# Kernel optimization log

Hardware: AMD Instinct MI355X
Metric: run time of the kernel (lower is better)

The kernel has to match this reference:

```python
import jax, jax.numpy as jnp
import numpy as np

I, H, O = 8, 32, 1  # input_size, hidden_size, output_size


def setup_inputs() -> dict:
    key = jax.random.key(0)
    ks = jax.random.split(key, 7)
    B, T = 4096, 256
    s_ih = 1.0 / np.sqrt(H)
    inp = {
        "x": jax.random.normal(ks[0], (B, T, I), dtype=jnp.float32),
        # PyTorch nn.LSTM params, gate order [i, f, g, o]
        "W_ih": jax.random.uniform(ks[1], (4 * H, I), minval=-s_ih, maxval=s_ih, dtype=jnp.float32),
        "W_hh": jax.random.uniform(ks[2], (4 * H, H), minval=-s_ih, maxval=s_ih, dtype=jnp.float32),
        "b_ih": jax.random.uniform(ks[3], (4 * H,), minval=-s_ih, maxval=s_ih, dtype=jnp.float32),
        "b_hh": jax.random.uniform(ks[4], (4 * H,), minval=-s_ih, maxval=s_ih, dtype=jnp.float32),
        # nn.Linear(H, O)
        "W_out": jax.random.uniform(ks[5], (O, H), minval=-s_ih, maxval=s_ih, dtype=jnp.float32),
        "b_out": jax.random.uniform(ks[6], (O,), minval=-s_ih, maxval=s_ih, dtype=jnp.float32),
    }
    return inp


def _lstm_last_h(x, W_ih, W_hh, b_ih, b_hh):
    B = x.shape[0]
    # Precompute input projections for all steps: [T, B, 4H]
    x_proj = jnp.einsum("bti,gi->tbg", x, W_ih) + (b_ih + b_hh)
    h0 = jnp.zeros((B, H), dtype=x.dtype)
    c0 = jnp.zeros((B, H), dtype=x.dtype)

    def step(carry, xp):
        h, c = carry
        z = xp + h @ W_hh.T  # [B, 4H]
        i = jax.nn.sigmoid(z[:, 0 * H:1 * H])
        f = jax.nn.sigmoid(z[:, 1 * H:2 * H])
        g = jnp.tanh(z[:, 2 * H:3 * H])
        o = jax.nn.sigmoid(z[:, 3 * H:4 * H])
        c = f * c + i * g
        h = o * jnp.tanh(c)
        return (h, c), None

    (hT, _), _ = jax.lax.scan(step, (h0, c0), x_proj)
    return hT  # equals out[:, -1, :] for unidirectional batch_first LSTM


def reference(x, W_ih, W_hh, b_ih, b_hh, W_out, b_out):
    hT = _lstm_last_h(x, W_ih, W_hh, b_ih, b_hh)
    return hT @ W_out.T + b_out  # [B, O]
```

## Files before the change

kernel.cpp:

```cpp
#include <hip/hip_runtime.h>


#define T_LEN 256
#define LOG2E 1.4426950408889634f

typedef short bf16x8 __attribute__((ext_vector_type(8)));
typedef float f32x4 __attribute__((ext_vector_type(4)));

static __device__ inline short f2bf_rne(float f) {
    union { float f; unsigned u; } v; v.f = f;
    unsigned u = v.u;
    return (short)((u + 0x7FFFu + ((u >> 16) & 1u)) >> 16);
}
static __device__ inline short f2bf_fast(float f) {
    union { float f; unsigned u; } v; v.f = f;
    return (short)((v.u + 0x8000u) >> 16);
}
static __device__ inline unsigned pack_bf2(float a, float b) {
    union { float f; unsigned u; } x, y; x.f = a; y.f = b;
    return ((x.u + 0x8000u) >> 16) | ((y.u + 0x8000u) & 0xFFFF0000u);
}
static __device__ inline float bf2f(short s) {
    union { unsigned u; float f; } v;
    v.u = ((unsigned)(unsigned short)s) << 16;
    return v.f;
}

__global__ __launch_bounds__(256) void lstm_kernel(
    const float* __restrict__ x, const float* __restrict__ W_ih,
    const float* __restrict__ W_hh, const float* __restrict__ b_ih,
    const float* __restrict__ b_hh, const float* __restrict__ W_out,
    const float* __restrict__ b_out, float* __restrict__ out)
{
    __shared__ __attribute__((aligned(16))) short h_lds[2][16 * 40];

    const int tid  = threadIdx.x;
    const int w    = tid >> 6;
    const int lane = tid & 63;
    const int L    = lane & 15;
    const int q    = lane >> 4;
    const int row0 = blockIdx.x * 16;

    bf16x8 whh[2], wih[2];
    f32x4  bias[2];
#pragma unroll
    for (int e = 0; e < 2; ++e) {
        const int   n = 32 * (L & 3) + 8 * (L >> 2) + 2 * w + e;
        const float s = ((L & 3) == 2 ? 2.f * LOG2E : LOG2E);
        const float* src = W_hh + n * 32 + q * 8;
        bf16x8 fr;
#pragma unroll
        for (int j = 0; j < 8; ++j) fr[j] = f2bf_rne(src[j] * s);
        whh[e] = fr;
        bf16x8 gr = (bf16x8){0,0,0,0,0,0,0,0};
        if (q == 0) {
            const float* s2 = W_ih + n * 8;
#pragma unroll
            for (int j = 0; j < 8; ++j) gr[j] = f2bf_rne(s2[j] * s);
        }
        wih[e] = gr;
        f32x4 bb;
#pragma unroll
        for (int r = 0; r < 4; ++r) {
            const int   nr = 32 * r + 8 * q + 2 * w + e;
            const float sr = (r == 2 ? 2.f * LOG2E : LOG2E);
            bb[r] = (b_ih[nr] + b_hh[nr]) * sr;
        }
        bias[e] = bb;
    }

    const float4* xv = (const float4*)x;
    const size_t  xb = (size_t)(row0 + L) * (T_LEN * 8 / 4);
    float4 xr0[2] = {{0,0,0,0},{0,0,0,0}}, xr1[2] = {{0,0,0,0},{0,0,0,0}};
    bf16x8 xf0 = (bf16x8){0,0,0,0,0,0,0,0};
    if (q == 0) {
        const float4 a = xv[xb + 0], b = xv[xb + 1];
        xf0[0] = f2bf_fast(a.x); xf0[1] = f2bf_fast(a.y);
        xf0[2] = f2bf_fast(a.z); xf0[3] = f2bf_fast(a.w);
        xf0[4] = f2bf_fast(b.x); xf0[5] = f2bf_fast(b.y);
        xf0[6] = f2bf_fast(b.z); xf0[7] = f2bf_fast(b.w);
        xr0[1] = xv[xb + 2]; xr1[1] = xv[xb + 3];
        xr0[0] = xv[xb + 4]; xr1[0] = xv[xb + 5];
    }

    f32x4 zx[2];
    zx[0] = __builtin_amdgcn_mfma_f32_16x16x32_bf16(wih[0], xf0, bias[0], 0, 0, 0);
    zx[1] = __builtin_amdgcn_mfma_f32_16x16x32_bf16(wih[1], xf0, bias[1], 0, 0, 0);

    bf16x8 hfrag = (bf16x8){0,0,0,0,0,0,0,0};
    float c0 = 0.f, c1 = 0.f;

#pragma unroll 2
    for (int t = 0; t < T_LEN; ++t) {
        const int nxt = (t + 1) & 1;

        const f32x4 a0 = __builtin_amdgcn_mfma_f32_16x16x32_bf16(whh[0], hfrag, zx[0], 0, 0, 0);
        const f32x4 a1 = __builtin_amdgcn_mfma_f32_16x16x32_bf16(whh[1], hfrag, zx[1], 0, 0, 0);

        float h0, h1;
        {
            const float ei = __builtin_amdgcn_exp2f(fminf(-a0[0], 40.f));
            const float ef = __builtin_amdgcn_exp2f(fminf(-a0[1], 40.f));
            const float eg = __builtin_amdgcn_exp2f(fminf(-a0[2], 40.f));
            const float eo = __builtin_amdgcn_exp2f(fminf(-a0[3], 40.f));
            const float fv = __builtin_amdgcn_rcpf(1.f + ef);
            const float ig = (1.f - eg) * __builtin_amdgcn_rcpf((1.f + ei) * (1.f + eg));
            c0 = fmaf(fv, c0, ig);
            const float ec = __builtin_amdgcn_exp2f(fminf(c0 * (-2.f * LOG2E), 40.f));
            h0 = (1.f - ec) * __builtin_amdgcn_rcpf((1.f + eo) * (1.f + ec));
        }
        {
            const float ei = __builtin_amdgcn_exp2f(fminf(-a1[0], 40.f));
            const float ef = __builtin_amdgcn_exp2f(fminf(-a1[1], 40.f));
            const float eg = __builtin_amdgcn_exp2f(fminf(-a1[2], 40.f));
            const float eo = __builtin_amdgcn_exp2f(fminf(-a1[3], 40.f));
            const float fv = __builtin_amdgcn_rcpf(1.f + ef);
            const float ig = (1.f - eg) * __builtin_amdgcn_rcpf((1.f + ei) * (1.f + eg));
            c1 = fmaf(fv, c1, ig);
            const float ec = __builtin_amdgcn_exp2f(fminf(c1 * (-2.f * LOG2E), 40.f));
            h1 = (1.f - ec) * __builtin_amdgcn_rcpf((1.f + eo) * (1.f + ec));
        }

        *(unsigned*)(&h_lds[nxt][L * 40 + 8 * q + 2 * w]) = pack_bf2(h0, h1);

        __builtin_amdgcn_fence(__ATOMIC_RELEASE, "workgroup", "local");
        __builtin_amdgcn_s_barrier();
        __builtin_amdgcn_fence(__ATOMIC_ACQUIRE, "workgroup", "local");

        hfrag = *(const bf16x8*)(&h_lds[nxt][L * 40 + q * 8]);

        {
            const float4 a = xr0[nxt], b = xr1[nxt];
            bf16x8 xf;
            xf[0] = f2bf_fast(a.x); xf[1] = f2bf_fast(a.y);
            xf[2] = f2bf_fast(a.z); xf[3] = f2bf_fast(a.w);
            xf[4] = f2bf_fast(b.x); xf[5] = f2bf_fast(b.y);
            xf[6] = f2bf_fast(b.z); xf[7] = f2bf_fast(b.w);
            zx[0] = __builtin_amdgcn_mfma_f32_16x16x32_bf16(wih[0], xf, bias[0], 0, 0, 0);
            zx[1] = __builtin_amdgcn_mfma_f32_16x16x32_bf16(wih[1], xf, bias[1], 0, 0, 0);
            if (q == 0) {
                int tn = t + 3; if (tn >= T_LEN) tn = T_LEN - 1;
                xr0[nxt] = xv[xb + (size_t)tn * 2];
                xr1[nxt] = xv[xb + (size_t)tn * 2 + 1];
            }
        }
    }

    if (tid < 16) {
        float s = b_out[0];
#pragma unroll
        for (int k = 0; k < 32; ++k) s = fmaf(bf2f(h_lds[0][tid * 40 + k]), W_out[k], s);
        out[row0 + tid] = s;
    }
}

extern "C" void kernel_launch(void* const* d_in, const int* in_sizes, int n_in,
                              void* d_out, int out_size, void* d_ws, size_t ws_size,
                              hipStream_t stream) {
    const float* x     = (const float*)d_in[0];
    const float* W_ih  = (const float*)d_in[1];
    const float* W_hh  = (const float*)d_in[2];
    const float* b_ih  = (const float*)d_in[3];
    const float* b_hh  = (const float*)d_in[4];
    const float* W_out = (const float*)d_in[5];
    const float* b_out = (const float*)d_in[6];
    float* out = (float*)d_out;

    const int B = in_sizes[0] / (T_LEN * 8);
    const int tiles = B / 16;
    lstm_kernel<<<tiles, 256, 0, stream>>>(x, W_ih, W_hh, b_ih, b_hh, W_out, b_out, out);
}
```

Measured before the change: 163.4 us.

## Stage x in LDS as bf16 halves and drop per-step global loads

```diff
diff --git a/kernel.cpp b/kernel.cpp
--- a/kernel.cpp
+++ b/kernel.cpp
@@ -1,20 +1,19 @@
 #include <hip/hip_runtime.h>
 
 
-#define T_LEN 256
-#define LOG2E 1.4426950408889634f
+#define T_LEN   256
+#define HALF_T  128
+#define XSTRIDE 130
+#define LOG2E   1.4426950408889634f
 
 typedef short bf16x8 __attribute__((ext_vector_type(8)));
-typedef float f32x4 __attribute__((ext_vector_type(4)));
+typedef float f32x4  __attribute__((ext_vector_type(4)));
+typedef unsigned u32x4 __attribute__((ext_vector_type(4)));
 
 static __device__ inline short f2bf_rne(float f) {
     union { float f; unsigned u; } v; v.f = f;
     unsigned u = v.u;
     return (short)((u + 0x7FFFu + ((u >> 16) & 1u)) >> 16);
-}
-static __device__ inline short f2bf_fast(float f) {
-    union { float f; unsigned u; } v; v.f = f;
-    return (short)((v.u + 0x8000u) >> 16);
 }
 static __device__ inline unsigned pack_bf2(float a, float b) {
     union { float f; unsigned u; } x, y; x.f = a; y.f = b;
@@ -32,6 +31,7 @@
     const float* __restrict__ b_hh, const float* __restrict__ W_out,
     const float* __restrict__ b_out, float* __restrict__ out)
 {
+    __shared__ __attribute__((aligned(16))) short xl[HALF_T * XSTRIDE];
     __shared__ __attribute__((aligned(16))) short h_lds[2][16 * 40];
 
     const int tid  = threadIdx.x;
@@ -40,6 +40,7 @@
     const int L    = lane & 15;
     const int q    = lane >> 4;
     const int row0 = blockIdx.x * 16;
+    const float4* xv = (const float4*)x;
 
     bf16x8 whh[2], wih[2];
     f32x4  bias[2];
@@ -69,40 +70,66 @@
         bias[e] = bb;
     }
 
-    const float4* xv = (const float4*)x;
-    const size_t  xb = (size_t)(row0 + L) * (T_LEN * 8 / 4);
-    float4 xr0[2] = {{0,0,0,0},{0,0,0,0}}, xr1[2] = {{0,0,0,0},{0,0,0,0}};
-    bf16x8 xf0 = (bf16x8){0,0,0,0,0,0,0,0};
-    if (q == 0) {
-        const float4 a = xv[xb + 0], b = xv[xb + 1];
-        xf0[0] = f2bf_fast(a.x); xf0[1] = f2bf_fast(a.y);
-        xf0[2] = f2bf_fast(a.z); xf0[3] = f2bf_fast(a.w);
-        xf0[4] = f2bf_fast(b.x); xf0[5] = f2bf_fast(b.y);
-        xf0[6] = f2bf_fast(b.z); xf0[7] = f2bf_fast(b.w);
-        xr0[1] = xv[xb + 2]; xr1[1] = xv[xb + 3];
-        xr0[0] = xv[xb + 4]; xr1[0] = xv[xb + 5];
+    for (int i = tid; i < 16 * 40; i += 256) h_lds[0][i] = 0;
+
+#pragma unroll
+    for (int it = 0; it < 8; ++it) {
+        const int idx = tid + (it << 8);
+        const int L2  = idx >> 7;
+        const int tl  = idx & (HALF_T - 1);
+        const float4* srcp = xv + ((size_t)(row0 + L2) * T_LEN + tl) * 2;
+        const float4 a = srcp[0], b = srcp[1];
+        u32x4 u;
+        u[0] = pack_bf2(a.x, a.y); u[1] = pack_bf2(a.z, a.w);
+        u[2] = pack_bf2(b.x, b.y); u[3] = pack_bf2(b.z, b.w);
+        *(u32x4*)(&xl[tl * XSTRIDE + L2 * 8]) = u;
+    }
+    __syncthreads();
+
+    f32x4 zx[2];
+    {
+        const bf16x8 xf0 = *(const bf16x8*)(&xl[L * 8]);
+        zx[0] = __builtin_amdgcn_mfma_f32_16x16x32_bf16(wih[0], xf0, bias[0], 0, 0, 0);
+        zx[1] = __builtin_amdgcn_mfma_f32_16x16x32_bf16(wih[1], xf0, bias[1], 0, 0, 0);
     }
 
-    f32x4 zx[2];
-    zx[0] = __builtin_amdgcn_mfma_f32_16x16x32_bf16(wih[0], xf0, bias[0], 0, 0, 0);
-    zx[1] = __builtin_amdgcn_mfma_f32_16x16x32_bf16(wih[1], xf0, bias[1], 0, 0, 0);
-
-    bf16x8 hfrag = (bf16x8){0,0,0,0,0,0,0,0};
     float c0 = 0.f, c1 = 0.f;
 
 #pragma unroll 2
     for (int t = 0; t < T_LEN; ++t) {
-        const int nxt = (t + 1) & 1;
+        if (t == HALF_T - 1) {
+#pragma unroll
+            for (int it = 0; it < 8; ++it) {
+                const int idx = tid + (it << 8);
+                const int L2  = idx >> 7;
+                const int tl  = idx & (HALF_T - 1);
+                const float4* srcp = xv + ((size_t)(row0 + L2) * T_LEN + HALF_T + tl) * 2;
+                const float4 a = srcp[0], b = srcp[1];
+                u32x4 u;
+                u[0] = pack_bf2(a.x, a.y); u[1] = pack_bf2(a.z, a.w);
+                u[2] = pack_bf2(b.x, b.y); u[3] = pack_bf2(b.z, b.w);
+                *(u32x4*)(&xl[tl * XSTRIDE + L2 * 8]) = u;
+            }
+            __syncthreads();
+        }
+
+        const int par = t & 1, nxt = par ^ 1;
+
+        const bf16x8 hfrag = *(const bf16x8*)(&h_lds[par][L * 40 + q * 8]);
+        int tn = t + 1; if (tn >= T_LEN) tn = T_LEN - 1;
+        const bf16x8 xfrag = *(const bf16x8*)(&xl[(tn & (HALF_T - 1)) * XSTRIDE + L * 8]);
 
         const f32x4 a0 = __builtin_amdgcn_mfma_f32_16x16x32_bf16(whh[0], hfrag, zx[0], 0, 0, 0);
         const f32x4 a1 = __builtin_amdgcn_mfma_f32_16x16x32_bf16(whh[1], hfrag, zx[1], 0, 0, 0);
+        zx[0] = __builtin_amdgcn_mfma_f32_16x16x32_bf16(wih[0], xfrag, bias[0], 0, 0, 0);
+        zx[1] = __builtin_amdgcn_mfma_f32_16x16x32_bf16(wih[1], xfrag, bias[1], 0, 0, 0);
 
         float h0, h1;
         {
-            const float ei = __builtin_amdgcn_exp2f(fminf(-a0[0], 40.f));
-            const float ef = __builtin_amdgcn_exp2f(fminf(-a0[1], 40.f));
-            const float eg = __builtin_amdgcn_exp2f(fminf(-a0[2], 40.f));
-            const float eo = __builtin_amdgcn_exp2f(fminf(-a0[3], 40.f));
+            const float ei = __builtin_amdgcn_exp2f(-a0[0]);
+            const float ef = __builtin_amdgcn_exp2f(-a0[1]);
+            const float eg = __builtin_amdgcn_exp2f(-a0[2]);
+            const float eo = __builtin_amdgcn_exp2f(-a0[3]);
             const float fv = __builtin_amdgcn_rcpf(1.f + ef);
             const float ig = (1.f - eg) * __builtin_amdgcn_rcpf((1.f + ei) * (1.f + eg));
             c0 = fmaf(fv, c0, ig);
@@ -110,10 +137,10 @@
             h0 = (1.f - ec) * __builtin_amdgcn_rcpf((1.f + eo) * (1.f + ec));
         }
         {
-            const float ei = __builtin_amdgcn_exp2f(fminf(-a1[0], 40.f));
-            const float ef = __builtin_amdgcn_exp2f(fminf(-a1[1], 40.f));
-            const float eg = __builtin_amdgcn_exp2f(fminf(-a1[2], 40.f));
-            const float eo = __builtin_amdgcn_exp2f(fminf(-a1[3], 40.f));
+            const float ei = __builtin_amdgcn_exp2f(-a1[0]);
+            const float ef = __builtin_amdgcn_exp2f(-a1[1]);
+            const float eg = __builtin_amdgcn_exp2f(-a1[2]);
+            const float eo = __builtin_amdgcn_exp2f(-a1[3]);
             const float fv = __builtin_amdgcn_rcpf(1.f + ef);
             const float ig = (1.f - eg) * __builtin_amdgcn_rcpf((1.f + ei) * (1.f + eg));
             c1 = fmaf(fv, c1, ig);
@@ -123,27 +150,7 @@
 
         *(unsigned*)(&h_lds[nxt][L * 40 + 8 * q + 2 * w]) = pack_bf2(h0, h1);
 
-        __builtin_amdgcn_fence(__ATOMIC_RELEASE, "workgroup", "local");
-        __builtin_amdgcn_s_barrier();
-        __builtin_amdgcn_fence(__ATOMIC_ACQUIRE, "workgroup", "local");
-
-        hfrag = *(const bf16x8*)(&h_lds[nxt][L * 40 + q * 8]);
-
-        {
-            const float4 a = xr0[nxt], b = xr1[nxt];
-            bf16x8 xf;
-            xf[0] = f2bf_fast(a.x); xf[1] = f2bf_fast(a.y);
-            xf[2] = f2bf_fast(a.z); xf[3] = f2bf_fast(a.w);
-            xf[4] = f2bf_fast(b.x); xf[5] = f2bf_fast(b.y);
-            xf[6] = f2bf_fast(b.z); xf[7] = f2bf_fast(b.w);
-            zx[0] = __builtin_amdgcn_mfma_f32_16x16x32_bf16(wih[0], xf, bias[0], 0, 0, 0);
-            zx[1] = __builtin_amdgcn_mfma_f32_16x16x32_bf16(wih[1], xf, bias[1], 0, 0, 0);
-            if (q == 0) {
-                int tn = t + 3; if (tn >= T_LEN) tn = T_LEN - 1;
-                xr0[nxt] = xv[xb + (size_t)tn * 2];
-                xr1[nxt] = xv[xb + (size_t)tn * 2 + 1];
-            }
-        }
+        __syncthreads();
     }
 
     if (tid < 16) {
```

Result: faster. 147.8 us (-9.6%).
